# Performance work log

Hardware: AMD Instinct MI355X
Metric: run time of the kernel (lower is better)

The kernel has to match this reference:

```python
import jax, jax.numpy as jnp
import numpy as np

B, S, D = 8, 512, 512
IN_S = IN_D = IN_E = 32
OUT_S = OUT_D = OUT_E = 32


def setup_inputs() -> dict:
    key = jax.random.key(0)
    ks = jax.random.split(key, 16)
    sc = 0.1
    return {
        "x_s": jax.random.normal(ks[0], (B, S, IN_S), jnp.float32),
        "x_d": jax.random.normal(ks[1], (B, D, IN_D), jnp.float32),
        "x_e": jax.random.normal(ks[2], (B, S, D, IN_E), jnp.float32),
        "W_ss": jax.random.normal(ks[3], (OUT_S, IN_S), jnp.float32) * sc,
        "b_ss": jnp.zeros((OUT_S,), jnp.float32),
        "W_se": jax.random.normal(ks[4], (OUT_S, IN_E), jnp.float32) * sc,
        "a_se_w": jax.random.normal(ks[5], (IN_E,), jnp.float32) * sc,
        "a_se_b": jnp.zeros((), jnp.float32),
        "W_dd": jax.random.normal(ks[6], (OUT_D, IN_D), jnp.float32) * sc,
        "b_dd": jnp.zeros((OUT_D,), jnp.float32),
        "W_de": jax.random.normal(ks[7], (OUT_D, IN_E), jnp.float32) * sc,
        "a_de_w": jax.random.normal(ks[8], (IN_E,), jnp.float32) * sc,
        "a_de_b": jnp.zeros((), jnp.float32),
        "W_ee": jax.random.normal(ks[9], (OUT_E, IN_E), jnp.float32) * sc,
        "b_ee": jnp.zeros((OUT_E,), jnp.float32),
        "W_es": jax.random.normal(ks[10], (OUT_E, IN_S), jnp.float32) * sc,
        "W_ed": jax.random.normal(ks[11], (OUT_E, IN_D), jnp.float32) * sc,
    }


def reference(x_s, x_d, x_e, W_ss, b_ss, W_se, a_se_w, a_se_b,
              W_dd, b_dd, W_de, a_de_w, a_de_b, W_ee, b_ee, W_es, W_ed):
    # Supply update: attention softmax over demand axis (dim=2)
    att_s = jax.nn.softmax(jnp.einsum('bsde,e->bsd', x_e, a_se_w) + a_se_b, axis=2)
    proj_se = jnp.einsum('bsde,oe->bsdo', x_e, W_se)
    h_s = jnp.einsum('bsi,oi->bso', x_s, W_ss) + b_ss \
        + jnp.einsum('bsdo,bsd->bso', proj_se, att_s)

    # Demand update: attention softmax over supply axis (dim=1)
    att_d = jax.nn.softmax(jnp.einsum('bsde,e->bsd', x_e, a_de_w) + a_de_b, axis=1)
    proj_de = jnp.einsum('bsde,oe->bsdo', x_e, W_de)
    h_d = jnp.einsum('bdi,oi->bdo', x_d, W_dd) + b_dd \
        + jnp.einsum('bsdo,bsd->bdo', proj_de, att_d)

    # Edge update: edge linear + broadcast node projections
    h_e = jnp.einsum('bsde,oe->bsdo', x_e, W_ee) + b_ee \
        + jnp.einsum('bsi,oi->bso', x_s, W_es)[:, :, None, :] \
        + jnp.einsum('bdi,oi->bdo', x_d, W_ed)[:, None, :, :]
    return (h_s, h_d, h_e)
```

## Files before the change

### kernel.cpp

```cpp
#include <hip/hip_runtime.h>
#include <cstddef>

#define B_ 8
#define S_ 512
#define D_ 512
#define TS 8
#define NST 64

#define WS_BASES 0
#define WS_PES   131072
#define WS_BASED 262144
#define WS_PED   393216
#define WS_UD    524288
#define WS_ZD    (WS_UD + B_*NST*D_*32)

#define HS_OFF 0
#define HD_OFF 131072
#define HE_OFF 262144

__global__ __launch_bounds__(256)
void k0_nodes(const float* __restrict__ x_s, const float* __restrict__ x_d,
              const float* __restrict__ W_ss, const float* __restrict__ b_ss,
              const float* __restrict__ W_dd, const float* __restrict__ b_dd,
              const float* __restrict__ W_es, const float* __restrict__ W_ed,
              float* __restrict__ ws)
{
  int g = blockIdx.x * 256 + threadIdx.x;
  int row = g >> 5, o = g & 31;
  bool sup = row < (B_ * S_);
  int r = sup ? row : row - B_ * S_;
  const float* x  = (sup ? x_s : x_d) + r * 32;
  const float* W1 = sup ? W_ss : W_dd;
  const float* W2 = sup ? W_es : W_ed;
  const float* bb = sup ? b_ss : b_dd;
  float xr[32];
#pragma unroll
  for (int k = 0; k < 8; k++)
    *(float4*)&xr[4*k] = *(const float4*)(x + 4*k);
  float acc1 = bb[o], acc2 = 0.f;
#pragma unroll
  for (int e = 0; e < 32; e++) {
    acc1 += xr[e] * W1[o*32 + e];
    acc2 += xr[e] * W2[o*32 + e];
  }
  int ob = sup ? WS_BASES : WS_BASED;
  int op = sup ? WS_PES  : WS_PED;
  ws[ob + r*32 + o] = acc1;
  ws[op + r*32 + o] = acc2;
}

__global__ __launch_bounds__(256, 2)
void k1_main(const float* __restrict__ x_e,
             const float* __restrict__ a_se_w, const float* __restrict__ a_se_b,
             const float* __restrict__ a_de_w, const float* __restrict__ a_de_b,
             const float* __restrict__ W_se, const float* __restrict__ W_ee,
             const float* __restrict__ b_ee,
             float* __restrict__ ws,
             float* __restrict__ out)
{
  __shared__ float lds_ud[D_ * 33];
  __shared__ float lds_us[TS * 32];
  __shared__ float lds_zs[TS];

  const int t = threadIdx.x;
  const int s_idx = t >> 5, d_off = t & 31;
  const int st = blockIdx.x, b = blockIdx.y;
  const int s = st * TS + s_idx;

  for (int idx = t; idx < D_ * 33; idx += 256) lds_ud[idx] = 0.f;
  if (t < TS) lds_zs[t] = 0.f;
  __syncthreads();

  const float* xrow  = x_e + ((size_t)(b * S_ + s) * D_) * 32;
  float*       herow = out + HE_OFF + ((size_t)(b * S_ + s) * D_) * 32;
  const float* peS = ws + WS_PES + (b * S_ + s) * 32;
  const float* peD = ws + WS_PED + (size_t)b * D_ * 32;

  float hbase[32];
#pragma unroll
  for (int k = 0; k < 8; k++) {
    float4 v  = *(const float4*)(peS + 4*k);
    float4 be = *(const float4*)(b_ee + 4*k);
    hbase[4*k+0] = v.x + be.x; hbase[4*k+1] = v.y + be.y;
    hbase[4*k+2] = v.z + be.z; hbase[4*k+3] = v.w + be.w;
  }

  float us_acc[32];
#pragma unroll
  for (int e = 0; e < 32; e++) us_acc[e] = 0.f;
  float zs_acc = 0.f;
  const float asb = a_se_b[0], adb = a_de_b[0];

  float4 xb[8];
#pragma unroll
  for (int k = 0; k < 8; k++)
    xb[k] = *(const float4*)(xrow + d_off*32 + 4*k);

#pragma unroll 1
  for (int i = 0; i < 16; i++) {
    const int d = i*32 + d_off;
    float x[32];
#pragma unroll
    for (int k = 0; k < 8; k++) {
      x[4*k+0] = xb[k].x; x[4*k+1] = xb[k].y;
      x[4*k+2] = xb[k].z; x[4*k+3] = xb[k].w;
    }
    const int dn = (i < 15) ? d + 32 : d;
#pragma unroll
    for (int k = 0; k < 8; k++)
      xb[k] = *(const float4*)(xrow + dn*32 + 4*k);

    float ls = asb, ldt = adb;
#pragma unroll
    for (int e = 0; e < 32; e++) {
      ls  += x[e] * a_se_w[e];
      ldt += x[e] * a_de_w[e];
    }
    float es = __expf(ls), ed = __expf(ldt);
    zs_acc += es;
#pragma unroll
    for (int e = 0; e < 32; e++) us_acc[e] += es * x[e];
#pragma unroll
    for (int e = 0; e < 32; e++)
      atomicAdd(&lds_ud[d*33 + e], ed * x[e]);
    atomicAdd(&lds_ud[d*33 + 32], ed);

#pragma unroll
    for (int oq = 0; oq < 8; oq++) {
      float4 pdq = *(const float4*)(peD + d*32 + 4*oq);
      float a0 = 0.f, a1 = 0.f, a2 = 0.f, a3 = 0.f;
#pragma unroll
      for (int e = 0; e < 32; e++) {
        a0 += x[e] * W_ee[(4*oq+0)*32 + e];
        a1 += x[e] * W_ee[(4*oq+1)*32 + e];
        a2 += x[e] * W_ee[(4*oq+2)*32 + e];
        a3 += x[e] * W_ee[(4*oq+3)*32 + e];
      }
      float4 r;
      r.x = a0 + hbase[4*oq+0] + pdq.x;
      r.y = a1 + hbase[4*oq+1] + pdq.y;
      r.z = a2 + hbase[4*oq+2] + pdq.z;
      r.w = a3 + hbase[4*oq+3] + pdq.w;
      *(float4*)(herow + d*32 + 4*oq) = r;
    }
  }

  atomicAdd(&lds_zs[s_idx], zs_acc);
  __syncthreads();

  float* wud = ws + WS_UD + ((size_t)(b * NST + st) * D_) * 32;
  float* wzd = ws + WS_ZD + (b * NST + st) * D_;
#pragma unroll 1
  for (int sw = 0; sw < 16; sw++) {
    int r = sw * 32 + (t >> 3), g = t & 7;
    *(float4*)(wud + r*32 + g*4) = *(float4*)&lds_ud[r*33 + g*4];
  }
  wzd[t]       = lds_ud[t*33 + 32];
  wzd[t + 256] = lds_ud[(t + 256)*33 + 32];
  __syncthreads();

  float* red = lds_ud;
#pragma unroll
  for (int k = 0; k < 8; k++) {
    float4 v;
    v.x = us_acc[4*k+0]; v.y = us_acc[4*k+1];
    v.z = us_acc[4*k+2]; v.w = us_acc[4*k+3];
    *(float4*)&red[t*33 + 4*k] = v;
  }
  __syncthreads();

  float sum = 0.f;
#pragma unroll 1
  for (int dd = 0; dd < 32; dd++)
    sum += red[(s_idx*32 + dd)*33 + d_off];
  lds_us[s_idx*32 + d_off] = sum / lds_zs[s_idx];
  __syncthreads();

  float acc = ws[WS_BASES + (b*S_ + s)*32 + d_off];
#pragma unroll
  for (int e = 0; e < 32; e++)
    acc += W_se[d_off*32 + e] * lds_us[s_idx*32 + e];
  out[HS_OFF + (b*S_ + s)*32 + d_off] = acc;
}

__global__ __launch_bounds__(256)
void k2_hd(const float* __restrict__ W_de, const float* __restrict__ ws,
           float* __restrict__ out)
{
  __shared__ float lds_u[8 * 32];
  const int t = threadIdx.x;
  const int r = t >> 5, e = t & 31;
  const int b = blockIdx.x >> 6, dg = blockIdx.x & 63;
  const int d = dg * 8 + r;
  const float* wud = ws + WS_UD;
  const float* wzd = ws + WS_ZD;
  float sum = 0.f, z = 0.f;
#pragma unroll 4
  for (int st = 0; st < NST; st++) {
    sum += wud[((size_t)(b*NST + st) * D_ + d) * 32 + e];
    z   += wzd[(b*NST + st) * D_ + d];
  }
  lds_u[r*32 + e] = sum / z;
  __syncthreads();
  float acc = ws[WS_BASED + (b*D_ + d)*32 + e];
#pragma unroll
  for (int ee = 0; ee < 32; ee++)
    acc += W_de[e*32 + ee] * lds_u[r*32 + ee];
  out[HD_OFF + (b*D_ + d)*32 + e] = acc;
}

extern "C" void kernel_launch(void* const* d_in, const int* in_sizes, int n_in,
                              void* d_out, int out_size, void* d_ws, size_t ws_size,
                              hipStream_t stream)
{
  const float* x_s    = (const float*)d_in[0];
  const float* x_d    = (const float*)d_in[1];
  const float* x_e    = (const float*)d_in[2];
  const float* W_ss   = (const float*)d_in[3];
  const float* b_ss   = (const float*)d_in[4];
  const float* W_se   = (const float*)d_in[5];
  const float* a_se_w = (const float*)d_in[6];
  const float* a_se_b = (const float*)d_in[7];
  const float* W_dd   = (const float*)d_in[8];
  const float* b_dd   = (const float*)d_in[9];
  const float* W_de   = (const float*)d_in[10];
  const float* a_de_w = (const float*)d_in[11];
  const float* a_de_b = (const float*)d_in[12];
  const float* W_ee   = (const float*)d_in[13];
  const float* b_ee   = (const float*)d_in[14];
  const float* W_es   = (const float*)d_in[15];
  const float* W_ed   = (const float*)d_in[16];
  float* out = (float*)d_out;
  float* ws  = (float*)d_ws;

  hipLaunchKernelGGL(k0_nodes, dim3(1024), dim3(256), 0, stream,
                     x_s, x_d, W_ss, b_ss, W_dd, b_dd, W_es, W_ed, ws);
  hipLaunchKernelGGL(k1_main, dim3(NST, B_), dim3(256), 0, stream,
                     x_e, a_se_w, a_se_b, a_de_w, a_de_b, W_se, W_ee, b_ee, ws, out);
  hipLaunchKernelGGL(k2_hd, dim3(512), dim3(256), 0, stream, W_de, ws, out);
}
```

Baseline: 770.3 us.

## Restructure edge kernel: per-thread demand ownership, LDS-staged coalesced tiles, atomic reductions

The main kernel now assigns each thread one demand column and loops over the block's supply rows. x_e rows and h_e rows go through a swizzled LDS tile so global loads and stores are fully coalesced. The demand-side softmax numerator now accumulates in registers and is flushed once per block with global atomics into a single buffer, replacing per-block partial buffers and the large LDS atomic array. That frees LDS for higher occupancy (4 blocks/CU) and lets one fused epilogue kernel compute h_s and h_d, with zeroing folded into the first kernel. The cost is extra barriers, LDS atomics for the supply sums, global float atomics (non-deterministic summation order), and reliance on the unnormalized exp staying in float range.

```diff
diff --git a/kernel.cpp b/kernel.cpp
--- a/kernel.cpp
+++ b/kernel.cpp
@@ -5,14 +5,17 @@
 #define S_ 512
 #define D_ 512
 #define TS 8
-#define NST 64
 
 #define WS_BASES 0
 #define WS_PES   131072
 #define WS_BASED 262144
 #define WS_PED   393216
 #define WS_UD    524288
-#define WS_ZD    (WS_UD + B_*NST*D_*32)
+#define WS_ZD    (WS_UD + B_*D_*32)
+#define WS_US    (WS_ZD + B_*D_)
+#define WS_ZS    (WS_US + B_*S_*32)
+#define WS_ZERO_BASE WS_UD
+#define WS_ZERO_F4   67584
 
 #define HS_OFF 0
 #define HD_OFF 131072
@@ -25,7 +28,14 @@
               const float* __restrict__ W_es, const float* __restrict__ W_ed,
               float* __restrict__ ws)
 {
-  int g = blockIdx.x * 256 + threadIdx.x;
+  const int blk = blockIdx.x, t = threadIdx.x;
+  if (blk >= 1024) {
+    int idx = (blk - 1024) * 256 + t;
+    if (idx < WS_ZERO_F4)
+      *(float4*)(ws + WS_ZERO_BASE + idx * 4) = make_float4(0.f, 0.f, 0.f, 0.f);
+    return;
+  }
+  int g = blk * 256 + t;
   int row = g >> 5, o = g & 31;
   bool sup = row < (B_ * S_);
   int r = sup ? row : row - B_ * S_;
@@ -43,91 +53,85 @@
     acc1 += xr[e] * W1[o*32 + e];
     acc2 += xr[e] * W2[o*32 + e];
   }
-  int ob = sup ? WS_BASES : WS_BASED;
-  int op = sup ? WS_PES  : WS_PED;
-  ws[ob + r*32 + o] = acc1;
-  ws[op + r*32 + o] = acc2;
-}
-
-__global__ __launch_bounds__(256, 2)
+  ws[(sup ? WS_BASES : WS_BASED) + r*32 + o] = acc1;
+  ws[(sup ? WS_PES   : WS_PED  ) + r*32 + o] = acc2;
+}
+
+__global__ __launch_bounds__(256, 4)
 void k1_main(const float* __restrict__ x_e,
              const float* __restrict__ a_se_w, const float* __restrict__ a_se_b,
              const float* __restrict__ a_de_w, const float* __restrict__ a_de_b,
-             const float* __restrict__ W_se, const float* __restrict__ W_ee,
-             const float* __restrict__ b_ee,
+             const float* __restrict__ W_ee, const float* __restrict__ b_ee,
              float* __restrict__ ws,
              float* __restrict__ out)
 {
-  __shared__ float lds_ud[D_ * 33];
-  __shared__ float lds_us[TS * 32];
-  __shared__ float lds_zs[TS];
+  __shared__ float tile[256 * 32];
+  __shared__ float us[TS * 33];
 
   const int t = threadIdx.x;
-  const int s_idx = t >> 5, d_off = t & 31;
-  const int st = blockIdx.x, b = blockIdx.y;
-  const int s = st * TS + s_idx;
-
-  for (int idx = t; idx < D_ * 33; idx += 256) lds_ud[idx] = 0.f;
-  if (t < TS) lds_zs[t] = 0.f;
+  const int st = blockIdx.x, half = blockIdx.y, b = blockIdx.z;
+  const int s0 = st * TS;
+  const int d_own = half * 256 + t;
+
+  for (int i = t; i < TS * 33; i += 256) us[i] = 0.f;
+
+  float pd[32];
+  const float* peD = ws + WS_PED + ((b * D_ + d_own) << 5);
+#pragma unroll
+  for (int k = 0; k < 8; k++)
+    *(float4*)&pd[4*k] = *(const float4*)(peD + 4*k);
+
+  float ud[32];
+#pragma unroll
+  for (int e = 0; e < 32; e++) ud[e] = 0.f;
+  float zd = 0.f;
+  const float asb = a_se_b[0], adb = a_de_b[0];
+
   __syncthreads();
 
-  const float* xrow  = x_e + ((size_t)(b * S_ + s) * D_) * 32;
-  float*       herow = out + HE_OFF + ((size_t)(b * S_ + s) * D_) * 32;
-  const float* peS = ws + WS_PES + (b * S_ + s) * 32;
-  const float* peD = ws + WS_PED + (size_t)b * D_ * 32;
-
-  float hbase[32];
-#pragma unroll
-  for (int k = 0; k < 8; k++) {
-    float4 v  = *(const float4*)(peS + 4*k);
-    float4 be = *(const float4*)(b_ee + 4*k);
-    hbase[4*k+0] = v.x + be.x; hbase[4*k+1] = v.y + be.y;
-    hbase[4*k+2] = v.z + be.z; hbase[4*k+3] = v.w + be.w;
-  }
-
-  float us_acc[32];
-#pragma unroll
-  for (int e = 0; e < 32; e++) us_acc[e] = 0.f;
-  float zs_acc = 0.f;
-  const float asb = a_se_b[0], adb = a_de_b[0];
-
-  float4 xb[8];
-#pragma unroll
-  for (int k = 0; k < 8; k++)
-    xb[k] = *(const float4*)(xrow + d_off*32 + 4*k);
-
 #pragma unroll 1
-  for (int i = 0; i < 16; i++) {
-    const int d = i*32 + d_off;
+  for (int si = 0; si < TS; si++) {
+    const int s = s0 + si;
+    const float* src = x_e + (((size_t)(b * S_ + s) * D_ + half * 256) << 5);
+
+#pragma unroll
+    for (int w = 0; w < 8; w++) {
+      const int g = w * 256 + t;
+      const int r = g >> 3, q = g & 7;
+      *(float4*)&tile[r*32 + ((q ^ (r & 7)) << 2)] = *(const float4*)(src + g*4);
+    }
+    __syncthreads();
+
     float x[32];
 #pragma unroll
-    for (int k = 0; k < 8; k++) {
-      x[4*k+0] = xb[k].x; x[4*k+1] = xb[k].y;
-      x[4*k+2] = xb[k].z; x[4*k+3] = xb[k].w;
-    }
-    const int dn = (i < 15) ? d + 32 : d;
-#pragma unroll
-    for (int k = 0; k < 8; k++)
-      xb[k] = *(const float4*)(xrow + dn*32 + 4*k);
-
-    float ls = asb, ldt = adb;
+    for (int q = 0; q < 8; q++)
+      *(float4*)&x[4*q] = *(const float4*)&tile[t*32 + ((q ^ (t & 7)) << 2)];
+
+    float ls = asb, ld2 = adb;
 #pragma unroll
     for (int e = 0; e < 32; e++) {
       ls  += x[e] * a_se_w[e];
-      ldt += x[e] * a_de_w[e];
-    }
-    float es = __expf(ls), ed = __expf(ldt);
-    zs_acc += es;
-#pragma unroll
-    for (int e = 0; e < 32; e++) us_acc[e] += es * x[e];
-#pragma unroll
-    for (int e = 0; e < 32; e++)
-      atomicAdd(&lds_ud[d*33 + e], ed * x[e]);
-    atomicAdd(&lds_ud[d*33 + 32], ed);
-
+      ld2 += x[e] * a_de_w[e];
+    }
+    float es = __expf(ls), ed = __expf(ld2);
+
+    zd += ed;
+#pragma unroll
+    for (int e = 0; e < 32; e++) ud[e] += ed * x[e];
+
+#pragma unroll
+    for (int k = 0; k < 32; k++) {
+      int e = (t + k) & 31;
+      atomicAdd(&us[si*33 + e], es * x[e]);
+    }
+    float v = es;
+#pragma unroll
+    for (int off = 32; off > 0; off >>= 1) v += __shfl_xor(v, off);
+    if ((t & 63) == 0) atomicAdd(&us[si*33 + 32], v);
+
+    const float* peS = ws + WS_PES + ((b * S_ + s) << 5);
 #pragma unroll
     for (int oq = 0; oq < 8; oq++) {
-      float4 pdq = *(const float4*)(peD + d*32 + 4*oq);
       float a0 = 0.f, a1 = 0.f, a2 = 0.f, a3 = 0.f;
 #pragma unroll
       for (int e = 0; e < 32; e++) {
@@ -136,77 +140,54 @@
         a2 += x[e] * W_ee[(4*oq+2)*32 + e];
         a3 += x[e] * W_ee[(4*oq+3)*32 + e];
       }
-      float4 r;
-      r.x = a0 + hbase[4*oq+0] + pdq.x;
-      r.y = a1 + hbase[4*oq+1] + pdq.y;
-      r.z = a2 + hbase[4*oq+2] + pdq.z;
-      r.w = a3 + hbase[4*oq+3] + pdq.w;
-      *(float4*)(herow + d*32 + 4*oq) = r;
-    }
-  }
-
-  atomicAdd(&lds_zs[s_idx], zs_acc);
-  __syncthreads();
-
-  float* wud = ws + WS_UD + ((size_t)(b * NST + st) * D_) * 32;
-  float* wzd = ws + WS_ZD + (b * NST + st) * D_;
-#pragma unroll 1
-  for (int sw = 0; sw < 16; sw++) {
-    int r = sw * 32 + (t >> 3), g = t & 7;
-    *(float4*)(wud + r*32 + g*4) = *(float4*)&lds_ud[r*33 + g*4];
-  }
-  wzd[t]       = lds_ud[t*33 + 32];
-  wzd[t + 256] = lds_ud[(t + 256)*33 + 32];
-  __syncthreads();
-
-  float* red = lds_ud;
-#pragma unroll
-  for (int k = 0; k < 8; k++) {
-    float4 v;
-    v.x = us_acc[4*k+0]; v.y = us_acc[4*k+1];
-    v.z = us_acc[4*k+2]; v.w = us_acc[4*k+3];
-    *(float4*)&red[t*33 + 4*k] = v;
-  }
-  __syncthreads();
-
-  float sum = 0.f;
-#pragma unroll 1
-  for (int dd = 0; dd < 32; dd++)
-    sum += red[(s_idx*32 + dd)*33 + d_off];
-  lds_us[s_idx*32 + d_off] = sum / lds_zs[s_idx];
-  __syncthreads();
-
-  float acc = ws[WS_BASES + (b*S_ + s)*32 + d_off];
-#pragma unroll
-  for (int e = 0; e < 32; e++)
-    acc += W_se[d_off*32 + e] * lds_us[s_idx*32 + e];
-  out[HS_OFF + (b*S_ + s)*32 + d_off] = acc;
+      float4 r4;
+      r4.x = a0 + b_ee[4*oq+0] + peS[4*oq+0] + pd[4*oq+0];
+      r4.y = a1 + b_ee[4*oq+1] + peS[4*oq+1] + pd[4*oq+1];
+      r4.z = a2 + b_ee[4*oq+2] + peS[4*oq+2] + pd[4*oq+2];
+      r4.w = a3 + b_ee[4*oq+3] + peS[4*oq+3] + pd[4*oq+3];
+      *(float4*)&tile[t*32 + ((oq ^ (t & 7)) << 2)] = r4;
+    }
+    __syncthreads();
+
+    float* dst = out + HE_OFF + (((size_t)(b * S_ + s) * D_ + half * 256) << 5);
+#pragma unroll
+    for (int w = 0; w < 8; w++) {
+      const int g = w * 256 + t;
+      const int r = g >> 3, q = g & 7;
+      *(float4*)(dst + g*4) = *(const float4*)&tile[r*32 + ((q ^ (r & 7)) << 2)];
+    }
+    __syncthreads();
+  }
+
+  float* udp = ws + WS_UD + ((b * D_ + d_own) << 5);
+#pragma unroll
+  for (int e = 0; e < 32; e++) atomicAdd(udp + e, ud[e]);
+  atomicAdd(ws + WS_ZD + b * D_ + d_own, zd);
+
+  for (int i = t; i < TS * 33; i += 256) {
+    int si = i / 33, j = i - si * 33;
+    int srow = b * S_ + s0 + si;
+    if (j < 32) atomicAdd(ws + WS_US + srow*32 + j, us[i]);
+    else        atomicAdd(ws + WS_ZS + srow, us[i]);
+  }
 }
 
 __global__ __launch_bounds__(256)
-void k2_hd(const float* __restrict__ W_de, const float* __restrict__ ws,
-           float* __restrict__ out)
-{
-  __shared__ float lds_u[8 * 32];
-  const int t = threadIdx.x;
-  const int r = t >> 5, e = t & 31;
-  const int b = blockIdx.x >> 6, dg = blockIdx.x & 63;
-  const int d = dg * 8 + r;
-  const float* wud = ws + WS_UD;
-  const float* wzd = ws + WS_ZD;
-  float sum = 0.f, z = 0.f;
-#pragma unroll 4
-  for (int st = 0; st < NST; st++) {
-    sum += wud[((size_t)(b*NST + st) * D_ + d) * 32 + e];
-    z   += wzd[(b*NST + st) * D_ + d];
-  }
-  lds_u[r*32 + e] = sum / z;
-  __syncthreads();
-  float acc = ws[WS_BASED + (b*D_ + d)*32 + e];
-#pragma unroll
-  for (int ee = 0; ee < 32; ee++)
-    acc += W_de[e*32 + ee] * lds_u[r*32 + ee];
-  out[HD_OFF + (b*D_ + d)*32 + e] = acc;
+void k2_epi(const float* __restrict__ W_se, const float* __restrict__ W_de,
+            const float* __restrict__ ws, float* __restrict__ out)
+{
+  int g = blockIdx.x * 256 + threadIdx.x;
+  int row = g >> 5, o = g & 31;
+  bool sup = row < B_ * S_;
+  int r = sup ? row : row - B_ * S_;
+  const float* u = ws + (sup ? WS_US : WS_UD) + r*32;
+  float z = ws[(sup ? WS_ZS : WS_ZD) + r];
+  const float* W = sup ? W_se : W_de;
+  float dot = 0.f;
+#pragma unroll
+  for (int e = 0; e < 32; e++) dot += W[o*32 + e] * u[e];
+  float base = ws[(sup ? WS_BASES : WS_BASED) + r*32 + o];
+  out[(sup ? HS_OFF : HD_OFF) + r*32 + o] = base + dot / z;
 }
 
 extern "C" void kernel_launch(void* const* d_in, const int* in_sizes, int n_in,
@@ -233,9 +214,10 @@
   float* out = (float*)d_out;
   float* ws  = (float*)d_ws;
 
-  hipLaunchKernelGGL(k0_nodes, dim3(1024), dim3(256), 0, stream,
+  hipLaunchKernelGGL(k0_nodes, dim3(1288), dim3(256), 0, stream,
                      x_s, x_d, W_ss, b_ss, W_dd, b_dd, W_es, W_ed, ws);
-  hipLaunchKernelGGL(k1_main, dim3(NST, B_), dim3(256), 0, stream,
-                     x_e, a_se_w, a_se_b, a_de_w, a_de_b, W_se, W_ee, b_ee, ws, out);
-  hipLaunchKernelGGL(k2_hd, dim3(512), dim3(256), 0, stream, W_de, ws, out);
-}
+  hipLaunchKernelGGL(k1_main, dim3(64, 2, B_), dim3(256), 0, stream,
+                     x_e, a_se_w, a_se_b, a_de_w, a_de_b, W_ee, b_ee, ws, out);
+  hipLaunchKernelGGL(k2_epi, dim3(1024), dim3(256), 0, stream,
+                     W_se, W_de, ws, out);
+}
```

Measured after the change: 1.459 ms. +89.3%, slower.
